# Kernel tuning notes

Measured on AMD Instinct MI355X. Metric: run time of the kernel, lower is better.

## Reference

```python
import jax, jax.numpy as jnp
import numpy as np

EMBED_DIM = 1024
N_HEADS = 16
HEAD_SIZE = EMBED_DIM // N_HEADS
SCALE = HEAD_SIZE ** -0.5


def setup_inputs() -> dict:
    key = jax.random.key(0)
    ks = jax.random.split(key, 11)
    B, Tq, Tk, C = 4, 1024, 1024, EMBED_DIM
    std = 0.02
    return {
        "q": jax.random.normal(ks[0], (B, Tq, C), jnp.float32),
        "k": jax.random.normal(ks[1], (B, Tk, C), jnp.float32),
        "v": jax.random.normal(ks[2], (B, Tk, C), jnp.float32),
        "Wq": jax.random.normal(ks[3], (C, C), jnp.float32) * std,
        "bq": jnp.zeros((C,), jnp.float32),
        "Wk": jax.random.normal(ks[4], (C, C), jnp.float32) * std,
        "bk": jnp.zeros((C,), jnp.float32),
        "Wv": jax.random.normal(ks[5], (C, C), jnp.float32) * std,
        "bv": jnp.zeros((C,), jnp.float32),
        "Wo": jax.random.normal(ks[6], (C, C), jnp.float32) * std,
        "bo": jnp.zeros((C,), jnp.float32),
    }


def reference(q, k, v, Wq, bq, Wk, bk, Wv, bv, Wo, bo):
    b, t, c = q.shape
    # linear projections (torch Linear: x @ W.T + b)
    qp = q @ Wq.T + bq            # [b, tq, c]
    kp = k @ Wk.T + bk            # [b, tk, c]
    vp = v @ Wv.T + bv            # [b, tk, c]
    # split heads: [b, h, t, d]
    qh = qp.reshape(b, t, N_HEADS, HEAD_SIZE).transpose(0, 2, 1, 3)
    kh = kp.reshape(b, kp.shape[1], N_HEADS, HEAD_SIZE).transpose(0, 2, 1, 3)
    vh = vp.reshape(b, vp.shape[1], N_HEADS, HEAD_SIZE).transpose(0, 2, 1, 3)
    # scaled dot-product attention
    scores = jnp.einsum('bhqd,bhkd->bhqk', qh, kh) * SCALE
    weights = jax.nn.softmax(scores, axis=-1)
    attn = jnp.einsum('bhqk,bhkd->bhqd', weights, vh)
    attn = attn.transpose(0, 2, 1, 3).reshape(b, t, c)
    out = attn @ Wo.T + bo
    return out
```

## Files before the change

kernel.cpp:

```cpp
#include <hip/hip_runtime.h>
#include <stdint.h>

typedef unsigned short u16;
typedef unsigned int   u32;
typedef __bf16 bf16;
typedef bf16  bf16x8 __attribute__((ext_vector_type(8)));
typedef float f32x4  __attribute__((ext_vector_type(4)));

#define AS1 __attribute__((address_space(1)))
#define AS3 __attribute__((address_space(3)))


__device__ __forceinline__ u16 f2bf(float f) {
  u32 u = __float_as_uint(f);
  return (u16)((u + 0x7fffu + ((u >> 16) & 1u)) >> 16);
}

__device__ __forceinline__ void gload_lds16(const void* src, void* dst) {
  __builtin_amdgcn_global_load_lds((const AS1 void*)src, (AS3 void*)dst, 16, 0, 0);
}

__device__ __forceinline__ bf16x8 fragL(const char* lds, int row, int kbyte) {
  return *(const bf16x8*)(lds + row * 128 + kbyte);
}


__global__ __launch_bounds__(256) void cvt_all(
    const float* q, const float* k, const float* v,
    const float* wq, const float* wk, const float* wv, const float* wo,
    u16* qb, u16* kb, u16* vb,
    u16* wqb, u16* wkb, u16* wvb, u16* wob)
{
  const float* src; u16* dst; int n4;
  switch (blockIdx.y) {
    case 0: src = q;  dst = qb;  n4 = 1048576; break;
    case 1: src = k;  dst = kb;  n4 = 1048576; break;
    case 2: src = v;  dst = vb;  n4 = 1048576; break;
    case 3: src = wq; dst = wqb; n4 = 262144;  break;
    case 4: src = wk; dst = wkb; n4 = 262144;  break;
    case 5: src = wv; dst = wvb; n4 = 262144;  break;
    default: src = wo; dst = wob; n4 = 262144; break;
  }
  int stride = gridDim.x * blockDim.x;
  for (int i = blockIdx.x * blockDim.x + threadIdx.x; i < n4; i += stride) {
    float4 f = ((const float4*)src)[i];
    ushort4 o;
    o.x = f2bf(f.x); o.y = f2bf(f.y); o.z = f2bf(f.z); o.w = f2bf(f.w);
    ((ushort4*)dst)[i] = o;
  }
}


__device__ __forceinline__ void stageL(const u16* gtile, char* lds, int tid)
{
  int w = tid >> 6, lane = tid & 63;
  int rr = lane >> 3;
  int cb = (lane & 7) << 4;
  #pragma unroll
  for (int i = 0; i < 4; ++i) {
    int c = i * 4 + w;
    gload_lds16((const char*)(gtile + (c * 8 + rr) * 1024) + cb, lds + c * 1024);
  }
}

__device__ __forceinline__ void gemm_core(const u16* A, const u16* W,
                                          f32x4 acc[4][4], int bi, int bj,
                                          int tid, char* As, char* Bs)
{
  int lane = tid & 63;
  int wr = (tid >> 7) & 1, wc = (tid >> 6) & 1;
  for (int kt = 0; kt < 16; ++kt) {
    stageL(A + bi * 128 * 1024 + kt * 64, As, tid);
    stageL(W + bj * 128 * 1024 + kt * 64, Bs, tid);
    __syncthreads();
    #pragma unroll
    for (int ks = 0; ks < 2; ++ks) {
      int kb = ks * 64 + ((lane >> 4) << 4);
      bf16x8 af[4], bfr[4];
      #pragma unroll
      for (int m = 0; m < 4; ++m) af[m]  = fragL(As, wr * 64 + m * 16 + (lane & 15), kb);
      #pragma unroll
      for (int n = 0; n < 4; ++n) bfr[n] = fragL(Bs, wc * 64 + n * 16 + (lane & 15), kb);
      #pragma unroll
      for (int m = 0; m < 4; ++m)
        #pragma unroll
        for (int n = 0; n < 4; ++n)
          acc[m][n] = __builtin_amdgcn_mfma_f32_16x16x32_bf16(af[m], bfr[n], acc[m][n], 0, 0, 0);
    }
    __syncthreads();
  }
}


__global__ __launch_bounds__(256, 2) void proj_gemm(
    const u16* qb, const u16* kb, const u16* vb,
    const u16* wqb, const u16* wkb, const u16* wvb,
    const float* bq, const float* bk, const float* bv,
    u16* qh, u16* kh, u16* vt)
{
  __shared__ alignas(16) char As[16384];
  __shared__ alignas(16) char Bs[16384];
  int tid = threadIdx.x;
  int bi = blockIdx.x & 31, bj = blockIdx.x >> 5;
  int z = blockIdx.z;
  const u16* A = (z == 0) ? qb : (z == 1) ? kb : vb;
  const u16* W = (z == 0) ? wqb : (z == 1) ? wkb : wvb;
  const float* bias = (z == 0) ? bq : (z == 1) ? bk : bv;
  u16* dst = (z == 0) ? qh : (z == 1) ? kh : vt;

  f32x4 acc[4][4] = {};
  gemm_core(A, W, acc, bi, bj, tid, As, Bs);

  int lane = tid & 63, wr = (tid >> 7) & 1, wc = (tid >> 6) & 1;
  int rbase = bi * 128 + wr * 64 + ((lane >> 4) << 2);
  int cbase = bj * 128 + wc * 64;
  #pragma unroll
  for (int n = 0; n < 4; ++n) {
    int col = cbase + n * 16 + (lane & 15);
    float bsv = bias[col];
    int h = col >> 6, d = col & 63;
    #pragma unroll
    for (int m = 0; m < 4; ++m) {
      #pragma unroll
      for (int r = 0; r < 4; ++r) {
        int R = rbase + m * 16 + r;
        int b = R >> 10, t = R & 1023;
        u16 val = f2bf(acc[m][n][r] + bsv);
        if (z < 2) dst[(((b * 16 + h) * 1024 + t) << 6) + d] = val;
        else       dst[(((b * 16 + h) * 64 + d) << 10) + t] = val;
      }
    }
  }
}


__global__ __launch_bounds__(256, 2) void out_gemm(
    const u16* attn, const u16* wob, const float* bo, float* out)
{
  __shared__ alignas(16) char As[16384];
  __shared__ alignas(16) char Bs[16384];
  int tid = threadIdx.x;
  int bi = blockIdx.x & 31, bj = blockIdx.x >> 5;

  f32x4 acc[4][4] = {};
  gemm_core(attn, wob, acc, bi, bj, tid, As, Bs);

  int lane = tid & 63, wr = (tid >> 7) & 1, wc = (tid >> 6) & 1;
  int rbase = bi * 128 + wr * 64 + ((lane >> 4) << 2);
  int cbase = bj * 128 + wc * 64;
  #pragma unroll
  for (int n = 0; n < 4; ++n) {
    int col = cbase + n * 16 + (lane & 15);
    float bsv = bo[col];
    #pragma unroll
    for (int m = 0; m < 4; ++m) {
      #pragma unroll
      for (int r = 0; r < 4; ++r) {
        int R = rbase + m * 16 + r;
        out[R * 1024 + col] = acc[m][n][r] + bsv;
      }
    }
  }
}


__global__ __launch_bounds__(256, 2) void attn_fwd(
    const u16* qh, const u16* kh, const u16* vt, u16* attnb)
{
  __shared__ alignas(16) u16 Ks[64 * 72];
  __shared__ alignas(16) u16 Vs[64 * 72];
  __shared__ alignas(16) u16 Pl[4][16 * 72];

  int tid = threadIdx.x, lane = tid & 63, w = tid >> 6;
  int g = lane >> 4;
  int q0 = blockIdx.x << 6;
  int bh = blockIdx.y;
  const u16* qbase = qh + bh * 65536;
  const u16* kbase = kh + bh * 65536;
  const u16* vbase = vt + bh * 65536;

  bf16x8 qf[2];
  {
    int qrow = q0 + w * 16 + (lane & 15);
    const u16* p = qbase + qrow * 64 + (g << 3);
    qf[0] = *(const bf16x8*)p;
    qf[1] = *(const bf16x8*)(p + 32);
  }

  f32x4 ot[4] = {};
  float m_r = -3.0e38f, l_r = 0.f;

  int sr = tid >> 2;
  int sj = (tid & 3) << 4;
  u16* pw = Pl[w];
  int prow = (lane & 15) * 72;

  for (int kv0 = 0; kv0 < 1024; kv0 += 64) {
    {
      const u16* ksrc = kbase + (kv0 + sr) * 64 + sj;
      const u16* vsrc = vbase + sr * 1024 + kv0 + sj;
      *(bf16x8*)(Ks + sr * 72 + sj)     = *(const bf16x8*)ksrc;
      *(bf16x8*)(Ks + sr * 72 + sj + 8) = *(const bf16x8*)(ksrc + 8);
      *(bf16x8*)(Vs + sr * 72 + sj)     = *(const bf16x8*)vsrc;
      *(bf16x8*)(Vs + sr * 72 + sj + 8) = *(const bf16x8*)(vsrc + 8);
    }
    __syncthreads();

    f32x4 sc[4] = {};
    #pragma unroll
    for (int ks = 0; ks < 2; ++ks) {
      #pragma unroll
      for (int m = 0; m < 4; ++m) {
        bf16x8 kf = *(const bf16x8*)(Ks + (m * 16 + (lane & 15)) * 72 + ks * 32 + g * 8);
        sc[m] = __builtin_amdgcn_mfma_f32_16x16x32_bf16(kf, qf[ks], sc[m], 0, 0, 0);
      }
    }

    float sv[4][4];
    float vmax = -3.0e38f;
    #pragma unroll
    for (int m = 0; m < 4; ++m)
      #pragma unroll
      for (int r = 0; r < 4; ++r) {
        sv[m][r] = sc[m][r] * 0.125f;
        vmax = fmaxf(vmax, sv[m][r]);
      }
    vmax = fmaxf(vmax, __shfl_xor(vmax, 16, 64));
    vmax = fmaxf(vmax, __shfl_xor(vmax, 32, 64));
    float mnew = fmaxf(m_r, vmax);
    float fac = __expf(m_r - mnew);
    float psum = 0.f;
    u32 pp[4][2];
    #pragma unroll
    for (int m = 0; m < 4; ++m) {
      float p0 = __expf(sv[m][0] - mnew);
      float p1 = __expf(sv[m][1] - mnew);
      float p2 = __expf(sv[m][2] - mnew);
      float p3 = __expf(sv[m][3] - mnew);
      psum += (p0 + p1) + (p2 + p3);
      pp[m][0] = (u32)f2bf(p0) | ((u32)f2bf(p1) << 16);
      pp[m][1] = (u32)f2bf(p2) | ((u32)f2bf(p3) << 16);
    }
    psum += __shfl_xor(psum, 16, 64);
    psum += __shfl_xor(psum, 32, 64);
    l_r = l_r * fac + psum;
    m_r = mnew;
    #pragma unroll
    for (int dm = 0; dm < 4; ++dm) ot[dm] *= fac;

    #pragma unroll
    for (int m = 0; m < 4; ++m) {
      u32* d = (u32*)(pw + prow + m * 16 + (g << 2));
      d[0] = pp[m][0];
      d[1] = pp[m][1];
    }

    #pragma unroll
    for (int ks = 0; ks < 2; ++ks) {
      bf16x8 pf = *(const bf16x8*)(pw + prow + ks * 32 + g * 8);
      #pragma unroll
      for (int dm = 0; dm < 4; ++dm) {
        bf16x8 vf = *(const bf16x8*)(Vs + (dm * 16 + (lane & 15)) * 72 + ks * 32 + g * 8);
        ot[dm] = __builtin_amdgcn_mfma_f32_16x16x32_bf16(vf, pf, ot[dm], 0, 0, 0);
      }
    }
    __syncthreads();
  }

  float inv = 1.0f / l_r;
  int b = bh >> 4, h = bh & 15;
  int tok = (b << 10) + q0 + w * 16 + (lane & 15);
  u16* obase = attnb + tok * 1024 + h * 64;
  #pragma unroll
  for (int dm = 0; dm < 4; ++dm) {
    int d0 = dm * 16 + (g << 2);
    u32 lo = (u32)f2bf(ot[dm][0] * inv) | ((u32)f2bf(ot[dm][1] * inv) << 16);
    u32 hi = (u32)f2bf(ot[dm][2] * inv) | ((u32)f2bf(ot[dm][3] * inv) << 16);
    u32* d = (u32*)(obase + d0);
    d[0] = lo; d[1] = hi;
  }
}


extern "C" void kernel_launch(void* const* d_in, const int* in_sizes, int n_in,
                              void* d_out, int out_size, void* d_ws, size_t ws_size,
                              hipStream_t stream)
{
  const float* q  = (const float*)d_in[0];
  const float* k  = (const float*)d_in[1];
  const float* v  = (const float*)d_in[2];
  const float* Wq = (const float*)d_in[3];
  const float* bq = (const float*)d_in[4];
  const float* Wk = (const float*)d_in[5];
  const float* bk = (const float*)d_in[6];
  const float* Wv = (const float*)d_in[7];
  const float* bv = (const float*)d_in[8];
  const float* Wo = (const float*)d_in[9];
  const float* bo = (const float*)d_in[10];
  float* out = (float*)d_out;

  u16* ws  = (u16*)d_ws;
  u16* qb  = ws;
  u16* kb  = qb  + (4u << 20);
  u16* vb  = kb  + (4u << 20);
  u16* wqb = vb  + (4u << 20);
  u16* wkb = wqb + (1u << 20);
  u16* wvb = wkb + (1u << 20);
  u16* wob = wvb + (1u << 20);
  u16* qhb = wob + (1u << 20);
  u16* khb = qhb + (4u << 20);
  u16* vtb = khb + (4u << 20);
  u16* atb = vtb + (4u << 20);

  cvt_all<<<dim3(1024, 7, 1), 256, 0, stream>>>(q, k, v, Wq, Wk, Wv, Wo,
                                                qb, kb, vb, wqb, wkb, wvb, wob);
  proj_gemm<<<dim3(256, 1, 3), 256, 0, stream>>>(qb, kb, vb, wqb, wkb, wvb,
                                                 bq, bk, bv, qhb, khb, vtb);
  attn_fwd<<<dim3(16, 64, 1), 256, 0, stream>>>(qhb, khb, vtb, atb);
  out_gemm<<<dim3(256, 1, 1), 256, 0, stream>>>(atb, wob, bo, out);
}
```

Baseline: 224.7 us.

## Fuse fp32-to-bf16 activation conversion into projection GEMM and lazily rescale softmax

Drops the separate conversion pass over q/k/v: the projection GEMM now loads fp32 activations and converts them to bf16 while staging into LDS, and only the weights are pre-converted. This removes a full write and re-read of 24M bf16 elements, but the A operand now goes through registers instead of direct global-to-LDS loads. The attention softmax skips rescaling the running max unless it grows past a threshold, folds the scale into an fma, and uses hardware bf16 packing conversions. The lazy rescale can let exp values grow large, which bf16 probabilities and fp32 sums must tolerate.

```diff
diff --git a/kernel.cpp b/kernel.cpp
--- a/kernel.cpp
+++ b/kernel.cpp
@@ -4,6 +4,7 @@
 typedef unsigned short u16;
 typedef unsigned int   u32;
 typedef __bf16 bf16;
+typedef bf16  bf16x2 __attribute__((ext_vector_type(2)));
 typedef bf16  bf16x8 __attribute__((ext_vector_type(8)));
 typedef float f32x4  __attribute__((ext_vector_type(4)));
 
@@ -11,9 +12,16 @@
 #define AS3 __attribute__((address_space(3)))
 
 
-__device__ __forceinline__ u16 f2bf(float f) {
-  u32 u = __float_as_uint(f);
-  return (u16)((u + 0x7fffu + ((u >> 16) & 1u)) >> 16);
+__device__ __forceinline__ u32 pk2(float lo, float hi) {
+  bf16x2 t;
+  t[0] = (bf16)lo;
+  t[1] = (bf16)hi;
+  return __builtin_bit_cast(u32, t);
+}
+
+__device__ __forceinline__ u16 b1(float f) {
+  bf16 t = (bf16)f;
+  return __builtin_bit_cast(u16, t);
 }
 
 __device__ __forceinline__ void gload_lds16(const void* src, void* dst) {
@@ -25,28 +33,25 @@
 }
 
 
-__global__ __launch_bounds__(256) void cvt_all(
-    const float* q, const float* k, const float* v,
+__global__ __launch_bounds__(256) void cvt_w(
     const float* wq, const float* wk, const float* wv, const float* wo,
-    u16* qb, u16* kb, u16* vb,
     u16* wqb, u16* wkb, u16* wvb, u16* wob)
 {
-  const float* src; u16* dst; int n4;
+  const float* src; u16* dst;
   switch (blockIdx.y) {
-    case 0: src = q;  dst = qb;  n4 = 1048576; break;
-    case 1: src = k;  dst = kb;  n4 = 1048576; break;
-    case 2: src = v;  dst = vb;  n4 = 1048576; break;
-    case 3: src = wq; dst = wqb; n4 = 262144;  break;
-    case 4: src = wk; dst = wkb; n4 = 262144;  break;
-    case 5: src = wv; dst = wvb; n4 = 262144;  break;
-    default: src = wo; dst = wob; n4 = 262144; break;
-  }
+    case 0: src = wq; dst = wqb; break;
+    case 1: src = wk; dst = wkb; break;
+    case 2: src = wv; dst = wvb; break;
+    default: src = wo; dst = wob; break;
+  }
+  const int n4 = 262144;
   int stride = gridDim.x * blockDim.x;
   for (int i = blockIdx.x * blockDim.x + threadIdx.x; i < n4; i += stride) {
     float4 f = ((const float4*)src)[i];
-    ushort4 o;
-    o.x = f2bf(f.x); o.y = f2bf(f.y); o.z = f2bf(f.z); o.w = f2bf(f.w);
-    ((ushort4*)dst)[i] = o;
+    uint2 o;
+    o.x = pk2(f.x, f.y);
+    o.y = pk2(f.z, f.w);
+    ((uint2*)dst)[i] = o;
   }
 }
 
@@ -63,37 +68,48 @@
   }
 }
 
-__device__ __forceinline__ void gemm_core(const u16* A, const u16* W,
-                                          f32x4 acc[4][4], int bi, int bj,
-                                          int tid, char* As, char* Bs)
-{
-  int lane = tid & 63;
-  int wr = (tid >> 7) & 1, wc = (tid >> 6) & 1;
-  for (int kt = 0; kt < 16; ++kt) {
-    stageL(A + bi * 128 * 1024 + kt * 64, As, tid);
-    stageL(W + bj * 128 * 1024 + kt * 64, Bs, tid);
-    __syncthreads();
-    #pragma unroll
-    for (int ks = 0; ks < 2; ++ks) {
-      int kb = ks * 64 + ((lane >> 4) << 4);
-      bf16x8 af[4], bfr[4];
-      #pragma unroll
-      for (int m = 0; m < 4; ++m) af[m]  = fragL(As, wr * 64 + m * 16 + (lane & 15), kb);
-      #pragma unroll
-      for (int n = 0; n < 4; ++n) bfr[n] = fragL(Bs, wc * 64 + n * 16 + (lane & 15), kb);
-      #pragma unroll
-      for (int m = 0; m < 4; ++m)
-        #pragma unroll
-        for (int n = 0; n < 4; ++n)
-          acc[m][n] = __builtin_amdgcn_mfma_f32_16x16x32_bf16(af[m], bfr[n], acc[m][n], 0, 0, 0);
-    }
-    __syncthreads();
+__device__ __forceinline__ void stageA_f32(const float* gA, char* lds, int tid)
+{
+  int r0 = tid >> 3;
+  int c8 = (tid & 7) << 3;
+  #pragma unroll
+  for (int i = 0; i < 4; ++i) {
+    int r = i * 32 + r0;
+    const float* p = gA + r * 1024 + c8;
+    float4 f0 = *(const float4*)p;
+    float4 f1 = *(const float4*)(p + 4);
+    uint4 o;
+    o.x = pk2(f0.x, f0.y);
+    o.y = pk2(f0.z, f0.w);
+    o.z = pk2(f1.x, f1.y);
+    o.w = pk2(f1.z, f1.w);
+    *(uint4*)(lds + r * 128 + (c8 << 1)) = o;
+  }
+}
+
+__device__ __forceinline__ void mfma_tile(const char* As, const char* Bs,
+                                          f32x4 acc[4][4], int lane,
+                                          int wr, int wc)
+{
+  #pragma unroll
+  for (int ks = 0; ks < 2; ++ks) {
+    int kb = ks * 64 + ((lane >> 4) << 4);
+    bf16x8 af[4], bfr[4];
+    #pragma unroll
+    for (int m = 0; m < 4; ++m) af[m]  = fragL(As, wr * 64 + m * 16 + (lane & 15), kb);
+    #pragma unroll
+    for (int n = 0; n < 4; ++n) bfr[n] = fragL(Bs, wc * 64 + n * 16 + (lane & 15), kb);
+    #pragma unroll
+    for (int m = 0; m < 4; ++m)
+      #pragma unroll
+      for (int n = 0; n < 4; ++n)
+        acc[m][n] = __builtin_amdgcn_mfma_f32_16x16x32_bf16(af[m], bfr[n], acc[m][n], 0, 0, 0);
   }
 }
 
 
 __global__ __launch_bounds__(256, 2) void proj_gemm(
-    const u16* qb, const u16* kb, const u16* vb,
+    const float* qf, const float* kf, const float* vf,
     const u16* wqb, const u16* wkb, const u16* wvb,
     const float* bq, const float* bk, const float* bv,
     u16* qh, u16* kh, u16* vt)
@@ -103,15 +119,22 @@
   int tid = threadIdx.x;
   int bi = blockIdx.x & 31, bj = blockIdx.x >> 5;
   int z = blockIdx.z;
-  const u16* A = (z == 0) ? qb : (z == 1) ? kb : vb;
+  const float* A = (z == 0) ? qf : (z == 1) ? kf : vf;
   const u16* W = (z == 0) ? wqb : (z == 1) ? wkb : wvb;
   const float* bias = (z == 0) ? bq : (z == 1) ? bk : bv;
   u16* dst = (z == 0) ? qh : (z == 1) ? kh : vt;
 
+  int lane = tid & 63;
+  int wr = (tid >> 7) & 1, wc = (tid >> 6) & 1;
   f32x4 acc[4][4] = {};
-  gemm_core(A, W, acc, bi, bj, tid, As, Bs);
-
-  int lane = tid & 63, wr = (tid >> 7) & 1, wc = (tid >> 6) & 1;
+  for (int kt = 0; kt < 16; ++kt) {
+    stageA_f32(A + bi * 131072 + kt * 64, As, tid);
+    stageL(W + bj * 131072 + kt * 64, Bs, tid);
+    __syncthreads();
+    mfma_tile(As, Bs, acc, lane, wr, wc);
+    __syncthreads();
+  }
+
   int rbase = bi * 128 + wr * 64 + ((lane >> 4) << 2);
   int cbase = bj * 128 + wc * 64;
   #pragma unroll
@@ -125,7 +148,7 @@
       for (int r = 0; r < 4; ++r) {
         int R = rbase + m * 16 + r;
         int b = R >> 10, t = R & 1023;
-        u16 val = f2bf(acc[m][n][r] + bsv);
+        u16 val = b1(acc[m][n][r] + bsv);
         if (z < 2) dst[(((b * 16 + h) * 1024 + t) << 6) + d] = val;
         else       dst[(((b * 16 + h) * 64 + d) << 10) + t] = val;
       }
@@ -142,10 +165,17 @@
   int tid = threadIdx.x;
   int bi = blockIdx.x & 31, bj = blockIdx.x >> 5;
 
+  int lane = tid & 63;
+  int wr = (tid >> 7) & 1, wc = (tid >> 6) & 1;
   f32x4 acc[4][4] = {};
-  gemm_core(attn, wob, acc, bi, bj, tid, As, Bs);
-
-  int lane = tid & 63, wr = (tid >> 7) & 1, wc = (tid >> 6) & 1;
+  for (int kt = 0; kt < 16; ++kt) {
+    stageL(attn + bi * 131072 + kt * 64, As, tid);
+    stageL(wob  + bj * 131072 + kt * 64, Bs, tid);
+    __syncthreads();
+    mfma_tile(As, Bs, acc, lane, wr, wc);
+    __syncthreads();
+  }
+
   int rbase = bi * 128 + wr * 64 + ((lane >> 4) << 2);
   int cbase = bj * 128 + wc * 64;
   #pragma unroll
@@ -170,6 +200,9 @@
   __shared__ alignas(16) u16 Ks[64 * 72];
   __shared__ alignas(16) u16 Vs[64 * 72];
   __shared__ alignas(16) u16 Pl[4][16 * 72];
+
+  const float SC = 0.125f;
+  const float RTHR = 64.0f;
 
   int tid = threadIdx.x, lane = tid & 63, w = tid >> 6;
   int g = lane >> 4;
@@ -216,37 +249,40 @@
       }
     }
 
-    float sv[4][4];
     float vmax = -3.0e38f;
     #pragma unroll
     for (int m = 0; m < 4; ++m)
       #pragma unroll
-      for (int r = 0; r < 4; ++r) {
-        sv[m][r] = sc[m][r] * 0.125f;
-        vmax = fmaxf(vmax, sv[m][r]);
-      }
+      for (int r = 0; r < 4; ++r)
+        vmax = fmaxf(vmax, sc[m][r]);
     vmax = fmaxf(vmax, __shfl_xor(vmax, 16, 64));
     vmax = fmaxf(vmax, __shfl_xor(vmax, 32, 64));
-    float mnew = fmaxf(m_r, vmax);
-    float fac = __expf(m_r - mnew);
+
+    if (!__all(vmax - m_r <= RTHR)) {
+      float mnew = fmaxf(m_r, vmax);
+      float fac = __expf((m_r - mnew) * SC);
+      l_r *= fac;
+      #pragma unroll
+      for (int dm = 0; dm < 4; ++dm) ot[dm] *= fac;
+      m_r = mnew;
+    }
+    float nm = -m_r * SC;
+
     float psum = 0.f;
     u32 pp[4][2];
     #pragma unroll
     for (int m = 0; m < 4; ++m) {
-      float p0 = __expf(sv[m][0] - mnew);
-      float p1 = __expf(sv[m][1] - mnew);
-      float p2 = __expf(sv[m][2] - mnew);
-      float p3 = __expf(sv[m][3] - mnew);
+      float p0 = __expf(fmaf(sc[m][0], SC, nm));
+      float p1 = __expf(fmaf(sc[m][1], SC, nm));
+      float p2 = __expf(fmaf(sc[m][2], SC, nm));
+      float p3 = __expf(fmaf(sc[m][3], SC, nm));
       psum += (p0 + p1) + (p2 + p3);
-      pp[m][0] = (u32)f2bf(p0) | ((u32)f2bf(p1) << 16);
-      pp[m][1] = (u32)f2bf(p2) | ((u32)f2bf(p3) << 16);
+      pp[m][0] = pk2(p0, p1);
+      pp[m][1] = pk2(p2, p3);
     }
     psum += __shfl_xor(psum, 16, 64);
     psum += __shfl_xor(psum, 32, 64);
-    l_r = l_r * fac + psum;
-    m_r = mnew;
-    #pragma unroll
-    for (int dm = 0; dm < 4; ++dm) ot[dm] *= fac;
+    l_r += psum;
 
     #pragma unroll
     for (int m = 0; m < 4; ++m) {
@@ -274,10 +310,9 @@
   #pragma unroll
   for (int dm = 0; dm < 4; ++dm) {
     int d0 = dm * 16 + (g << 2);
-    u32 lo = (u32)f2bf(ot[dm][0] * inv) | ((u32)f2bf(ot[dm][1] * inv) << 16);
-    u32 hi = (u32)f2bf(ot[dm][2] * inv) | ((u32)f2bf(ot[dm][3] * inv) << 16);
     u32* d = (u32*)(obase + d0);
-    d[0] = lo; d[1] = hi;
+    d[0] = pk2(ot[dm][0] * inv, ot[dm][1] * inv);
+    d[1] = pk2(ot[dm][2] * inv, ot[dm][3] * inv);
   }
 }
 
@@ -300,10 +335,7 @@
   float* out = (float*)d_out;
 
   u16* ws  = (u16*)d_ws;
-  u16* qb  = ws;
-  u16* kb  = qb  + (4u << 20);
-  u16* vb  = kb  + (4u << 20);
-  u16* wqb = vb  + (4u << 20);
+  u16* wqb = ws;
   u16* wkb = wqb + (1u << 20);
   u16* wvb = wkb + (1u << 20);
   u16* wob = wvb + (1u << 20);
@@ -312,9 +344,8 @@
   u16* vtb = khb + (4u << 20);
   u16* atb = vtb + (4u << 20);
 
-  cvt_all<<<dim3(1024, 7, 1), 256, 0, stream>>>(q, k, v, Wq, Wk, Wv, Wo,
-                                                qb, kb, vb, wqb, wkb, wvb, wob);
-  proj_gemm<<<dim3(256, 1, 3), 256, 0, stream>>>(qb, kb, vb, wqb, wkb, wvb,
+  cvt_w<<<dim3(256, 4, 1), 256, 0, stream>>>(Wq, Wk, Wv, Wo, wqb, wkb, wvb, wob);
+  proj_gemm<<<dim3(256, 1, 3), 256, 0, stream>>>(q, k, v, wqb, wkb, wvb,
                                                  bq, bk, bv, qhb, khb, vtb);
   attn_fwd<<<dim3(16, 64, 1), 256, 0, stream>>>(qhb, khb, vtb, atb);
   out_gemm<<<dim3(256, 1, 1), 256, 0, stream>>>(atb, wob, bo, out);
```

Measured after the change: 238.5 us. +6.1%, slower.
